# Kernel optimization log

Hardware: AMD Instinct MI355X
Metric: run time of the kernel (lower is better)

The kernel has to match this reference:

```python
import jax, jax.numpy as jnp
import numpy as np

K = 128
HEADS = 8
B = 4
T = 2048


def setup_inputs() -> dict:
    key = jax.random.key(0)
    ks = jax.random.split(key, 6)
    x = jax.random.normal(ks[0], (B, T, K), dtype=jnp.float32)
    s = 1.0 / np.sqrt(K)
    # torch nn.Linear weights are (out_features, in_features)
    Wq = jax.random.uniform(ks[1], (HEADS * K, K), dtype=jnp.float32, minval=-s, maxval=s)
    Wk = jax.random.uniform(ks[2], (HEADS * K, K), dtype=jnp.float32, minval=-s, maxval=s)
    Wv = jax.random.uniform(ks[3], (HEADS * K, K), dtype=jnp.float32, minval=-s, maxval=s)
    su = 1.0 / np.sqrt(HEADS * K)
    Wu = jax.random.uniform(ks[4], (K, HEADS * K), dtype=jnp.float32, minval=-su, maxval=su)
    bu = jax.random.uniform(ks[5], (K,), dtype=jnp.float32, minval=-su, maxval=su)
    return {"x": x, "Wq": Wq, "Wk": Wk, "Wv": Wv, "Wu": Wu, "bu": bu}


def reference(x, Wq, Wk, Wv, Wu, bu):
    b, t, k = x.shape
    h = HEADS
    # project: Linear(k, k*h) then view(b,t,h,k); weight reshaped to (h, k_out, k_in)
    q = jnp.einsum('btk,hdk->bhtd', x, Wq.reshape(h, k, k))
    kk = jnp.einsum('btk,hdk->bhtd', x, Wk.reshape(h, k, k))
    v = jnp.einsum('btk,hdk->bhtd', x, Wv.reshape(h, k, k))
    scale = jnp.asarray(k, x.dtype) ** 0.25
    q = q / scale
    kk = kk / scale
    dot = jnp.einsum('bhtd,bhsd->bhts', q, kk)  # [b,h,t,t]
    att = jax.nn.softmax(dot, axis=-1)
    out = jnp.einsum('bhts,bhsd->bhtd', att, v)  # [b,h,t,k]
    out = out.transpose(0, 2, 1, 3).reshape(b, t, h * k)
    return out @ Wu.T + bu
```

## Files before the change

kernel.cpp:

```cpp
#include <hip/hip_runtime.h>
#include <cmath>

namespace {

constexpr int HEADS = 8;
constexpr int Bn = 4;
constexpr int Tn = 2048;
constexpr int Dn = 128;
constexpr float Q_PRESCALE = 0.1275174340f;

typedef _Float16 half8 __attribute__((ext_vector_type(8)));
typedef _Float16 half4 __attribute__((ext_vector_type(4)));
typedef float f32x4 __attribute__((ext_vector_type(4)));

__global__ __launch_bounds__(256) void cast_kernel(
    const float* __restrict__ x, const float* __restrict__ Wq, const float* __restrict__ Wk,
    const float* __restrict__ Wv, const float* __restrict__ Wu, _Float16* __restrict__ xh,
    _Float16* __restrict__ WH) {
  const int idx = blockIdx.x * 256 + threadIdx.x;
  const size_t base = (size_t)idx * 8;
  const float* src;
  _Float16* dst;
  if (base < 1048576) {
    src = x + base;
    dst = xh + base;
  } else {
    const size_t r = base - 1048576;
    const int s = (int)(r >> 17);
    src = ((s == 0) ? Wq : (s == 1) ? Wk : (s == 2) ? Wv : Wu) + (r & 131071);
    dst = WH + r;
  }
  const float4 a = *reinterpret_cast<const float4*>(src);
  const float4 b = *reinterpret_cast<const float4*>(src + 4);
  half8 h;
  h[0] = (_Float16)a.x; h[1] = (_Float16)a.y; h[2] = (_Float16)a.z; h[3] = (_Float16)a.w;
  h[4] = (_Float16)b.x; h[5] = (_Float16)b.y; h[6] = (_Float16)b.z; h[7] = (_Float16)b.w;
  *reinterpret_cast<half8*>(dst) = h;
}

__global__ __launch_bounds__(256, 4) void proj_kernel(const _Float16* __restrict__ xh,
                                                      const _Float16* __restrict__ WH,
                                                      _Float16* __restrict__ Qh,
                                                      _Float16* __restrict__ Kh,
                                                      _Float16* __restrict__ Vt) {
  __shared__ _Float16 sB[128 * 136];
  const int tid = threadIdx.x;
  const int w = tid >> 6, lane = tid & 63, quad = lane >> 4, l16 = lane & 15;
  const int m0 = blockIdx.x * 128;
  const int n0 = blockIdx.y * 128;

#pragma unroll
  for (int it = 0; it < 8; ++it) {
    const int fid = tid + it * 256;
    const int r = fid >> 4, g = fid & 15;
    const half8 v = *reinterpret_cast<const half8*>(WH + (size_t)(n0 + r) * 128 + g * 8);
    const int p = g ^ (r & 15);
    *reinterpret_cast<half8*>(sB + r * 128 + p * 8) = v;
  }

  half8 af[2][4];
  const _Float16* xp = xh + (size_t)(m0 + w * 32 + l16) * 128 + quad * 8;
#pragma unroll
  for (int mt = 0; mt < 2; ++mt)
#pragma unroll
    for (int kk = 0; kk < 4; ++kk)
      af[mt][kk] = *reinterpret_cast<const half8*>(xp + mt * 16 * 128 + kk * 32);

  __syncthreads();

  f32x4 acc[2][8];
#pragma unroll
  for (int mt = 0; mt < 2; ++mt)
#pragma unroll
    for (int nt = 0; nt < 8; ++nt) acc[mt][nt] = (f32x4){0.f, 0.f, 0.f, 0.f};

#pragma unroll
  for (int kk = 0; kk < 4; ++kk)
#pragma unroll
    for (int nt = 0; nt < 8; ++nt) {
      const int r = nt * 16 + l16;
      const int p = (kk * 4 + quad) ^ l16;
      const half8 bf = *reinterpret_cast<const half8*>(sB + r * 128 + p * 8);
      acc[0][nt] = __builtin_amdgcn_mfma_f32_16x16x32_f16(af[0][kk], bf, acc[0][nt], 0, 0, 0);
      acc[1][nt] = __builtin_amdgcn_mfma_f32_16x16x32_f16(af[1][kk], bf, acc[1][nt], 0, 0, 0);
    }

  const int sel = n0 >> 10;
  const int h = (n0 >> 7) & 7;
  const int b = m0 >> 11;
  const int t0b = m0 & 2047;
  const int bh = b * HEADS + h;
  const float scale = (sel == 0) ? Q_PRESCALE : 1.0f;

  __syncthreads();

  if (sel < 2) {
#pragma unroll
    for (int mt = 0; mt < 2; ++mt)
#pragma unroll
      for (int nt = 0; nt < 8; ++nt)
#pragma unroll
        for (int r = 0; r < 4; ++r)
          sB[(w * 32 + mt * 16 + quad * 4 + r) * 136 + nt * 16 + l16] =
              (_Float16)(acc[mt][nt][r] * scale);
  } else {
#pragma unroll
    for (int mt = 0; mt < 2; ++mt)
#pragma unroll
      for (int nt = 0; nt < 8; ++nt)
#pragma unroll
        for (int r = 0; r < 4; ++r)
          sB[(nt * 16 + l16) * 136 + w * 32 + mt * 16 + quad * 4 + r] = (_Float16)acc[mt][nt][r];
  }
  __syncthreads();

  _Float16* dstbase;
  size_t rstride;
  if (sel == 0) {
    dstbase = Qh + ((size_t)bh * Tn + t0b) * Dn;
    rstride = Dn;
  } else if (sel == 1) {
    dstbase = Kh + ((size_t)bh * Tn + t0b) * Dn;
    rstride = Dn;
  } else {
    dstbase = Vt + ((size_t)bh * Dn) * Tn + t0b;
    rstride = Tn;
  }
#pragma unroll
  for (int it = 0; it < 8; ++it) {
    const int fid = tid + it * 256;
    const int r = fid >> 4, g = fid & 15;
    const half8 v = *reinterpret_cast<const half8*>(sB + r * 136 + g * 8);
    *reinterpret_cast<half8*>(dstbase + (size_t)r * rstride + g * 8) = v;
  }
}

__global__ __launch_bounds__(256, 2) void flash_kernel(const _Float16* __restrict__ Qh,
                                                       const _Float16* __restrict__ Kh,
                                                       const _Float16* __restrict__ Vt,
                                                       _Float16* __restrict__ Obh) {
  __shared__ _Float16 sK[2][64 * 128];
  __shared__ _Float16 sV[2][128 * 64];
  __shared__ _Float16 sP[4][32 * 64];

  const int tid = threadIdx.x;
  const int w = tid >> 6;
  const int lane = tid & 63;
  const int quad = lane >> 4;
  const int l16 = lane & 15;
  const int qt = blockIdx.x;
  const int bh = blockIdx.y;
  constexpr int NT = Tn / 64;

  half8 qf[2][4];
#pragma unroll
  for (int qg = 0; qg < 2; ++qg) {
    const _Float16* Qp =
        Qh + ((size_t)bh * Tn + qt * 128 + w * 32 + qg * 16 + l16) * Dn + quad * 8;
#pragma unroll
    for (int kk = 0; kk < 4; ++kk) qf[qg][kk] = *reinterpret_cast<const half8*>(Qp + kk * 32);
  }

  const _Float16* Kp = Kh + (size_t)bh * Tn * Dn;
  const _Float16* Vp = Vt + (size_t)bh * Dn * Tn;
  _Float16* sPw = sP[w];

  f32x4 o[2][8];
#pragma unroll
  for (int qg = 0; qg < 2; ++qg)
#pragma unroll
    for (int nt = 0; nt < 8; ++nt) o[qg][nt] = (f32x4){0.f, 0.f, 0.f, 0.f};
  float lsum[2] = {0.f, 0.f};

  half8 kreg[4], vreg[4];
  const int kr = tid >> 4, kg = tid & 15;
  const int vr = tid >> 3, vg = tid & 7;

#pragma unroll
  for (int it = 0; it < 4; ++it) {
    kreg[it] = *reinterpret_cast<const half8*>(Kp + (size_t)(kr + it * 16) * Dn + kg * 8);
    vreg[it] = *reinterpret_cast<const half8*>(Vp + (size_t)(vr + it * 32) * Tn + vg * 8);
  }
#pragma unroll
  for (int it = 0; it < 4; ++it) {
    const int r = kr + it * 16;
    const int p = kg ^ (r & 15);
    *reinterpret_cast<half8*>(sK[0] + r * 128 + p * 8) = kreg[it];
    const int rv = vr + it * 32;
    const int pv = vg ^ ((rv & 7) ^ ((rv >> 1) & 4));
    *reinterpret_cast<half8*>(sV[0] + rv * 64 + pv * 8) = vreg[it];
  }
#pragma unroll
  for (int it = 0; it < 4; ++it) {
    kreg[it] = *reinterpret_cast<const half8*>(Kp + (size_t)(64 + kr + it * 16) * Dn + kg * 8);
    vreg[it] = *reinterpret_cast<const half8*>(Vp + (size_t)(vr + it * 32) * Tn + 64 + vg * 8);
  }
  __syncthreads();

  f32x4 s_t[2][4];
#pragma unroll
  for (int qg = 0; qg < 2; ++qg)
#pragma unroll
    for (int j = 0; j < 4; ++j) s_t[qg][j] = (f32x4){0.f, 0.f, 0.f, 0.f};
#pragma unroll
  for (int kk = 0; kk < 4; ++kk)
#pragma unroll
    for (int j = 0; j < 4; ++j) {
      const int p = (kk * 4 + quad) ^ l16;
      const half8 kf = *reinterpret_cast<const half8*>(sK[0] + (j * 16 + l16) * 128 + p * 8);
      s_t[0][j] = __builtin_amdgcn_mfma_f32_16x16x32_f16(kf, qf[0][kk], s_t[0][j], 0, 0, 0);
      s_t[1][j] = __builtin_amdgcn_mfma_f32_16x16x32_f16(kf, qf[1][kk], s_t[1][j], 0, 0, 0);
    }

  for (int st = 0; st < NT; ++st) {
    const int cur = st & 1, nxt = cur ^ 1;

    if (st + 1 < NT) {
#pragma unroll
      for (int it = 0; it < 4; ++it) {
        const int r = kr + it * 16;
        const int p = kg ^ (r & 15);
        *reinterpret_cast<half8*>(sK[nxt] + r * 128 + p * 8) = kreg[it];
        const int rv = vr + it * 32;
        const int pv = vg ^ ((rv & 7) ^ ((rv >> 1) & 4));
        *reinterpret_cast<half8*>(sV[nxt] + rv * 64 + pv * 8) = vreg[it];
      }
    }
    if (st + 2 < NT) {
      const _Float16* knext = Kp + (size_t)(st + 2) * 64 * Dn;
      const _Float16* vnext = Vp + (st + 2) * 64;
#pragma unroll
      for (int it = 0; it < 4; ++it) {
        kreg[it] = *reinterpret_cast<const half8*>(knext + (size_t)(kr + it * 16) * Dn + kg * 8);
        vreg[it] = *reinterpret_cast<const half8*>(vnext + (size_t)(vr + it * 32) * Tn + vg * 8);
      }
    }

#pragma unroll
    for (int h = 0; h < 2; ++h) {
#pragma unroll
      for (int qg = 0; qg < 2; ++qg)
#pragma unroll
        for (int jj = 0; jj < 2; ++jj) {
          const int j = h * 2 + jj;
          f32x4 e;
          e[0] = __builtin_amdgcn_exp2f(s_t[qg][j][0]);
          e[1] = __builtin_amdgcn_exp2f(s_t[qg][j][1]);
          e[2] = __builtin_amdgcn_exp2f(s_t[qg][j][2]);
          e[3] = __builtin_amdgcn_exp2f(s_t[qg][j][3]);
          lsum[qg] += (e[0] + e[1]) + (e[2] + e[3]);
          half4 h4;
          h4[0] = (_Float16)e[0]; h4[1] = (_Float16)e[1];
          h4[2] = (_Float16)e[2]; h4[3] = (_Float16)e[3];
          const int g = j * 2 + (quad >> 1);
          const int p = g ^ (l16 & 7);
          *reinterpret_cast<half4*>(sPw + (qg * 16 + l16) * 64 + p * 8 + (quad & 1) * 4) = h4;
        }
      half8 pf[2];
#pragma unroll
      for (int qg = 0; qg < 2; ++qg) {
        const int pA = (h * 4 + quad) ^ (l16 & 7);
        pf[qg] = *reinterpret_cast<const half8*>(sPw + (qg * 16 + l16) * 64 + pA * 8);
      }
#pragma unroll
      for (int nt = 0; nt < 8; ++nt) {
        const int r = nt * 16 + l16;
        const int pV = (h * 4 + quad) ^ ((r & 7) ^ ((r >> 1) & 4));
        const half8 vf = *reinterpret_cast<const half8*>(sV[cur] + r * 64 + pV * 8);
        o[0][nt] = __builtin_amdgcn_mfma_f32_16x16x32_f16(pf[0], vf, o[0][nt], 0, 0, 0);
        o[1][nt] = __builtin_amdgcn_mfma_f32_16x16x32_f16(pf[1], vf, o[1][nt], 0, 0, 0);
      }
    }

    __syncthreads();

    if (st + 1 < NT) {
#pragma unroll
      for (int qg = 0; qg < 2; ++qg)
#pragma unroll
        for (int j = 0; j < 4; ++j) s_t[qg][j] = (f32x4){0.f, 0.f, 0.f, 0.f};
#pragma unroll
      for (int kk = 0; kk < 4; ++kk)
#pragma unroll
        for (int j = 0; j < 4; ++j) {
          const int p = (kk * 4 + quad) ^ l16;
          const half8 kf =
              *reinterpret_cast<const half8*>(sK[nxt] + (j * 16 + l16) * 128 + p * 8);
          s_t[0][j] = __builtin_amdgcn_mfma_f32_16x16x32_f16(kf, qf[0][kk], s_t[0][j], 0, 0, 0);
          s_t[1][j] = __builtin_amdgcn_mfma_f32_16x16x32_f16(kf, qf[1][kk], s_t[1][j], 0, 0, 0);
        }
    }
  }

  float* sLw = reinterpret_cast<float*>(sPw);
#pragma unroll
  for (int qg = 0; qg < 2; ++qg) {
    float ls = lsum[qg];
    ls += __shfl_xor(ls, 16);
    ls += __shfl_xor(ls, 32);
    if (quad == 0) sLw[qg * 16 + l16] = 1.0f / ls;
  }
  const int b = bh >> 3, h = bh & 7;
#pragma unroll
  for (int qg = 0; qg < 2; ++qg) {
    const f32x4 inv4 = *reinterpret_cast<const f32x4*>(sLw + qg * 16 + quad * 4);
#pragma unroll
    for (int r = 0; r < 4; ++r) {
      const size_t trow =
          (size_t)(b * Tn + qt * 128 + w * 32 + qg * 16 + quad * 4 + r) * (HEADS * Dn);
#pragma unroll
      for (int nt = 0; nt < 8; ++nt)
        Obh[trow + h * Dn + nt * 16 + l16] = (_Float16)(o[qg][nt][r] * inv4[r]);
    }
  }
}

__global__ __launch_bounds__(256, 4) void outproj_kernel(const _Float16* __restrict__ Obh,
                                                         const _Float16* __restrict__ Wuh,
                                                         const float* __restrict__ bu,
                                                         float* __restrict__ out) {
  __shared__ float sR[4 * 32 * 128];
  const int tid = threadIdx.x;
  const int w = tid >> 6, lane = tid & 63, quad = lane >> 4, l16 = lane & 15;
  const int r0 = blockIdx.x * 32;

  f32x4 acc[2][8];
#pragma unroll
  for (int mt = 0; mt < 2; ++mt)
#pragma unroll
    for (int nt = 0; nt < 8; ++nt) acc[mt][nt] = (f32x4){0.f, 0.f, 0.f, 0.f};

  const _Float16* ap = Obh + (size_t)(r0 + l16) * 1024 + w * 256 + quad * 8;
  const _Float16* bp = Wuh + (size_t)l16 * 1024 + w * 256 + quad * 8;

#pragma unroll
  for (int kk = 0; kk < 8; ++kk) {
    const half8 a0 = *reinterpret_cast<const half8*>(ap + kk * 32);
    const half8 a1 = *reinterpret_cast<const half8*>(ap + 16 * 1024 + kk * 32);
#pragma unroll
    for (int nt = 0; nt < 8; ++nt) {
      const half8 bf = *reinterpret_cast<const half8*>(bp + (size_t)nt * 16 * 1024 + kk * 32);
      acc[0][nt] = __builtin_amdgcn_mfma_f32_16x16x32_f16(a0, bf, acc[0][nt], 0, 0, 0);
      acc[1][nt] = __builtin_amdgcn_mfma_f32_16x16x32_f16(a1, bf, acc[1][nt], 0, 0, 0);
    }
  }

#pragma unroll
  for (int mt = 0; mt < 2; ++mt)
#pragma unroll
    for (int nt = 0; nt < 8; ++nt)
#pragma unroll
      for (int r = 0; r < 4; ++r)
        sR[w * 4096 + (mt * 16 + quad * 4 + r) * 128 + nt * 16 + l16] = acc[mt][nt][r];
  __syncthreads();

#pragma unroll
  for (int it = 0; it < 16; ++it) {
    const int idx = tid + it * 256;
    const int row = idx >> 7, col = idx & 127;
    const float v = sR[idx] + sR[4096 + idx] + sR[8192 + idx] + sR[12288 + idx] + bu[col];
    out[(size_t)(r0 + row) * Dn + col] = v;
  }
}

}

extern "C" void kernel_launch(void* const* d_in, const int* in_sizes, int n_in, void* d_out,
                              int out_size, void* d_ws, size_t ws_size, hipStream_t stream) {
  (void)in_sizes; (void)n_in; (void)out_size; (void)ws_size;
  const float* x = (const float*)d_in[0];
  const float* Wq = (const float*)d_in[1];
  const float* Wk = (const float*)d_in[2];
  const float* Wv = (const float*)d_in[3];
  const float* Wu = (const float*)d_in[4];
  const float* bu = (const float*)d_in[5];
  float* out = (float*)d_out;

  constexpr size_t NE = (size_t)Bn * HEADS * Tn * Dn;
  char* ws = (char*)d_ws;
  _Float16* xh = (_Float16*)ws;
  _Float16* WH = (_Float16*)(ws + 2097152);
  _Float16* Qh = (_Float16*)(ws + 4194304);
  _Float16* Kh = (_Float16*)(ws + 4194304 + NE * 2);
  _Float16* Vt = (_Float16*)(ws + 4194304 + NE * 4);
  _Float16* Obh = (_Float16*)(ws + 4194304 + NE * 6);
  _Float16* Wuh = WH + 393216;

  cast_kernel<<<dim3(768), 256, 0, stream>>>(x, Wq, Wk, Wv, Wu, xh, WH);
  proj_kernel<<<dim3(64, 24), 256, 0, stream>>>(xh, WH, Qh, Kh, Vt);
  flash_kernel<<<dim3(16, 32), 256, 0, stream>>>(Qh, Kh, Vt, Obh);
  outproj_kernel<<<dim3(256), 256, 0, stream>>>(Obh, Wuh, bu, out);
}
```

Before: 168.5 us.

## Switch flash attention to 32x32 MFMA with register-resident P and larger Q tiles

Rewrites the flash attention kernel to use 32x32x16 MFMA instead of 16x16x32. Each wave now owns 64 query rows (256 per block), so the grid halves to 256 blocks. The softmax probabilities are packed straight into MFMA B-operand registers, which removes the LDS round trip for P. The output is staged through swizzled LDS so it can be written to global memory as coalesced 16-byte stores. In exchange there is more register pressure (launch bounds drop to one block per SM) and fewer blocks to hide latency, which could cost occupancy and load balance on a large GPU.

```diff
diff --git a/kernel.cpp b/kernel.cpp
--- a/kernel.cpp
+++ b/kernel.cpp
@@ -11,7 +11,11 @@
 
 typedef _Float16 half8 __attribute__((ext_vector_type(8)));
 typedef _Float16 half4 __attribute__((ext_vector_type(4)));
+typedef _Float16 half2v __attribute__((ext_vector_type(2)));
 typedef float f32x4 __attribute__((ext_vector_type(4)));
+typedef float f32x16 __attribute__((ext_vector_type(16)));
+typedef unsigned int u32;
+typedef unsigned int u32x4 __attribute__((ext_vector_type(4)));
 
 __global__ __launch_bounds__(256) void cast_kernel(
     const float* __restrict__ x, const float* __restrict__ Wq, const float* __restrict__ Wk,
@@ -135,60 +139,68 @@
   }
 }
 
-__global__ __launch_bounds__(256, 2) void flash_kernel(const _Float16* __restrict__ Qh,
+__global__ __launch_bounds__(256, 1) void flash_kernel(const _Float16* __restrict__ Qh,
                                                        const _Float16* __restrict__ Kh,
                                                        const _Float16* __restrict__ Vt,
                                                        _Float16* __restrict__ Obh) {
-  __shared__ _Float16 sK[2][64 * 128];
-  __shared__ _Float16 sV[2][128 * 64];
-  __shared__ _Float16 sP[4][32 * 64];
+  __shared__ _Float16 sAll[32768];
 
   const int tid = threadIdx.x;
   const int w = tid >> 6;
   const int lane = tid & 63;
-  const int quad = lane >> 4;
-  const int l16 = lane & 15;
+  const int l31 = lane & 31;
+  const int h = lane >> 5;
   const int qt = blockIdx.x;
   const int bh = blockIdx.y;
   constexpr int NT = Tn / 64;
 
-  half8 qf[2][4];
-#pragma unroll
-  for (int qg = 0; qg < 2; ++qg) {
+  half8 qf[2][8];
+#pragma unroll
+  for (int qb = 0; qb < 2; ++qb) {
     const _Float16* Qp =
-        Qh + ((size_t)bh * Tn + qt * 128 + w * 32 + qg * 16 + l16) * Dn + quad * 8;
-#pragma unroll
-    for (int kk = 0; kk < 4; ++kk) qf[qg][kk] = *reinterpret_cast<const half8*>(Qp + kk * 32);
+        Qh + ((size_t)bh * Tn + qt * 256 + w * 64 + qb * 32 + l31) * Dn + h * 8;
+#pragma unroll
+    for (int ds = 0; ds < 8; ++ds) qf[qb][ds] = *reinterpret_cast<const half8*>(Qp + ds * 16);
   }
 
   const _Float16* Kp = Kh + (size_t)bh * Tn * Dn;
   const _Float16* Vp = Vt + (size_t)bh * Dn * Tn;
-  _Float16* sPw = sP[w];
-
-  f32x4 o[2][8];
-#pragma unroll
-  for (int qg = 0; qg < 2; ++qg)
-#pragma unroll
-    for (int nt = 0; nt < 8; ++nt) o[qg][nt] = (f32x4){0.f, 0.f, 0.f, 0.f};
+
+  f32x16 o[4][2];
+#pragma unroll
+  for (int db = 0; db < 4; ++db)
+#pragma unroll
+    for (int qb = 0; qb < 2; ++qb) o[db][qb] = (f32x16)(0.f);
   float lsum[2] = {0.f, 0.f};
 
   half8 kreg[4], vreg[4];
   const int kr = tid >> 4, kg = tid & 15;
   const int vr = tid >> 3, vg = tid & 7;
+  const int vG = (vg >> 1) * 2;
+  const int vO = (vg & 1) * 4;
 
 #pragma unroll
   for (int it = 0; it < 4; ++it) {
     kreg[it] = *reinterpret_cast<const half8*>(Kp + (size_t)(kr + it * 16) * Dn + kg * 8);
     vreg[it] = *reinterpret_cast<const half8*>(Vp + (size_t)(vr + it * 32) * Tn + vg * 8);
   }
-#pragma unroll
-  for (int it = 0; it < 4; ++it) {
-    const int r = kr + it * 16;
-    const int p = kg ^ (r & 15);
-    *reinterpret_cast<half8*>(sK[0] + r * 128 + p * 8) = kreg[it];
-    const int rv = vr + it * 32;
-    const int pv = vg ^ ((rv & 7) ^ ((rv >> 1) & 4));
-    *reinterpret_cast<half8*>(sV[0] + rv * 64 + pv * 8) = vreg[it];
+  {
+    _Float16* sK0 = sAll;
+    _Float16* sV0 = sAll + 16384;
+#pragma unroll
+    for (int it = 0; it < 4; ++it) {
+      const int r = kr + it * 16;
+      const int p = kg ^ (r & 15);
+      *reinterpret_cast<half8*>(sK0 + r * 128 + p * 8) = kreg[it];
+      const int rv = vr + it * 32;
+      const int sw = (rv & 7) ^ ((rv >> 1) & 4);
+      const half8 v = vreg[it];
+      half4 lo, hi;
+      lo[0] = v[0]; lo[1] = v[1]; lo[2] = v[2]; lo[3] = v[3];
+      hi[0] = v[4]; hi[1] = v[5]; hi[2] = v[6]; hi[3] = v[7];
+      *reinterpret_cast<half4*>(sV0 + rv * 64 + ((vG ^ sw) * 8) + vO) = lo;
+      *reinterpret_cast<half4*>(sV0 + rv * 64 + (((vG + 1) ^ sw) * 8) + vO) = hi;
+    }
   }
 #pragma unroll
   for (int it = 0; it < 4; ++it) {
@@ -197,33 +209,48 @@
   }
   __syncthreads();
 
-  f32x4 s_t[2][4];
-#pragma unroll
-  for (int qg = 0; qg < 2; ++qg)
-#pragma unroll
-    for (int j = 0; j < 4; ++j) s_t[qg][j] = (f32x4){0.f, 0.f, 0.f, 0.f};
-#pragma unroll
-  for (int kk = 0; kk < 4; ++kk)
-#pragma unroll
-    for (int j = 0; j < 4; ++j) {
-      const int p = (kk * 4 + quad) ^ l16;
-      const half8 kf = *reinterpret_cast<const half8*>(sK[0] + (j * 16 + l16) * 128 + p * 8);
-      s_t[0][j] = __builtin_amdgcn_mfma_f32_16x16x32_f16(kf, qf[0][kk], s_t[0][j], 0, 0, 0);
-      s_t[1][j] = __builtin_amdgcn_mfma_f32_16x16x32_f16(kf, qf[1][kk], s_t[1][j], 0, 0, 0);
-    }
+  f32x16 sacc[2][2];
+#pragma unroll
+  for (int qb = 0; qb < 2; ++qb)
+#pragma unroll
+    for (int kb = 0; kb < 2; ++kb) sacc[qb][kb] = (f32x16)(0.f);
+#pragma unroll
+  for (int ds = 0; ds < 8; ++ds) {
+    half8 kf[2];
+#pragma unroll
+    for (int kb = 0; kb < 2; ++kb) {
+      const int r = kb * 32 + l31;
+      const int p = (ds * 2 + h) ^ (r & 15);
+      kf[kb] = *reinterpret_cast<const half8*>(sAll + r * 128 + p * 8);
+    }
+#pragma unroll
+    for (int qb = 0; qb < 2; ++qb)
+#pragma unroll
+      for (int kb = 0; kb < 2; ++kb)
+        sacc[qb][kb] =
+            __builtin_amdgcn_mfma_f32_32x32x16_f16(kf[kb], qf[qb][ds], sacc[qb][kb], 0, 0, 0);
+  }
 
   for (int st = 0; st < NT; ++st) {
     const int cur = st & 1, nxt = cur ^ 1;
+    _Float16* sKn = sAll + nxt * 8192;
+    _Float16* sVn = sAll + 16384 + nxt * 8192;
+    _Float16* sVc = sAll + 16384 + cur * 8192;
 
     if (st + 1 < NT) {
 #pragma unroll
       for (int it = 0; it < 4; ++it) {
         const int r = kr + it * 16;
         const int p = kg ^ (r & 15);
-        *reinterpret_cast<half8*>(sK[nxt] + r * 128 + p * 8) = kreg[it];
+        *reinterpret_cast<half8*>(sKn + r * 128 + p * 8) = kreg[it];
         const int rv = vr + it * 32;
-        const int pv = vg ^ ((rv & 7) ^ ((rv >> 1) & 4));
-        *reinterpret_cast<half8*>(sV[nxt] + rv * 64 + pv * 8) = vreg[it];
+        const int sw = (rv & 7) ^ ((rv >> 1) & 4);
+        const half8 v = vreg[it];
+        half4 lo, hi;
+        lo[0] = v[0]; lo[1] = v[1]; lo[2] = v[2]; lo[3] = v[3];
+        hi[0] = v[4]; hi[1] = v[5]; hi[2] = v[6]; hi[3] = v[7];
+        *reinterpret_cast<half4*>(sVn + rv * 64 + ((vG ^ sw) * 8) + vO) = lo;
+        *reinterpret_cast<half4*>(sVn + rv * 64 + (((vG + 1) ^ sw) * 8) + vO) = hi;
       }
     }
     if (st + 2 < NT) {
@@ -236,39 +263,38 @@
       }
     }
 
-#pragma unroll
-    for (int h = 0; h < 2; ++h) {
-#pragma unroll
-      for (int qg = 0; qg < 2; ++qg)
-#pragma unroll
-        for (int jj = 0; jj < 2; ++jj) {
-          const int j = h * 2 + jj;
-          f32x4 e;
-          e[0] = __builtin_amdgcn_exp2f(s_t[qg][j][0]);
-          e[1] = __builtin_amdgcn_exp2f(s_t[qg][j][1]);
-          e[2] = __builtin_amdgcn_exp2f(s_t[qg][j][2]);
-          e[3] = __builtin_amdgcn_exp2f(s_t[qg][j][3]);
-          lsum[qg] += (e[0] + e[1]) + (e[2] + e[3]);
-          half4 h4;
-          h4[0] = (_Float16)e[0]; h4[1] = (_Float16)e[1];
-          h4[2] = (_Float16)e[2]; h4[3] = (_Float16)e[3];
-          const int g = j * 2 + (quad >> 1);
-          const int p = g ^ (l16 & 7);
-          *reinterpret_cast<half4*>(sPw + (qg * 16 + l16) * 64 + p * 8 + (quad & 1) * 4) = h4;
+    half8 bfr[2][4];
+#pragma unroll
+    for (int qb = 0; qb < 2; ++qb) {
+#pragma unroll
+      for (int kb = 0; kb < 2; ++kb) {
+        u32 pk[8];
+        float part = 0.f;
+#pragma unroll
+        for (int j = 0; j < 8; ++j) {
+          const float e0 = __builtin_amdgcn_exp2f(sacc[qb][kb][2 * j]);
+          const float e1 = __builtin_amdgcn_exp2f(sacc[qb][kb][2 * j + 1]);
+          part += e0 + e1;
+          half2v hp = {(_Float16)e0, (_Float16)e1};
+          pk[j] = __builtin_bit_cast(u32, hp);
         }
-      half8 pf[2];
-#pragma unroll
-      for (int qg = 0; qg < 2; ++qg) {
-        const int pA = (h * 4 + quad) ^ (l16 & 7);
-        pf[qg] = *reinterpret_cast<const half8*>(sPw + (qg * 16 + l16) * 64 + pA * 8);
-      }
-#pragma unroll
-      for (int nt = 0; nt < 8; ++nt) {
-        const int r = nt * 16 + l16;
-        const int pV = (h * 4 + quad) ^ ((r & 7) ^ ((r >> 1) & 4));
-        const half8 vf = *reinterpret_cast<const half8*>(sV[cur] + r * 64 + pV * 8);
-        o[0][nt] = __builtin_amdgcn_mfma_f32_16x16x32_f16(pf[0], vf, o[0][nt], 0, 0, 0);
-        o[1][nt] = __builtin_amdgcn_mfma_f32_16x16x32_f16(pf[1], vf, o[1][nt], 0, 0, 0);
+        lsum[qb] += part;
+        u32x4 beven = {pk[0], pk[1], pk[2], pk[3]};
+        u32x4 bodd = {pk[4], pk[5], pk[6], pk[7]};
+        bfr[qb][kb * 2] = __builtin_bit_cast(half8, beven);
+        bfr[qb][kb * 2 + 1] = __builtin_bit_cast(half8, bodd);
+      }
+    }
+
+#pragma unroll
+    for (int kb16 = 0; kb16 < 4; ++kb16) {
+#pragma unroll
+      for (int db = 0; db < 4; ++db) {
+        const int r = db * 32 + l31;
+        const int pv = (kb16 * 2 + h) ^ ((r & 7) ^ ((r >> 1) & 4));
+        const half8 vf = *reinterpret_cast<const half8*>(sVc + r * 64 + pv * 8);
+        o[db][0] = __builtin_amdgcn_mfma_f32_32x32x16_f16(vf, bfr[0][kb16], o[db][0], 0, 0, 0);
+        o[db][1] = __builtin_amdgcn_mfma_f32_32x32x16_f16(vf, bfr[1][kb16], o[db][1], 0, 0, 0);
       }
     }
 
@@ -276,46 +302,66 @@
 
     if (st + 1 < NT) {
 #pragma unroll
-      for (int qg = 0; qg < 2; ++qg)
-#pragma unroll
-        for (int j = 0; j < 4; ++j) s_t[qg][j] = (f32x4){0.f, 0.f, 0.f, 0.f};
-#pragma unroll
-      for (int kk = 0; kk < 4; ++kk)
-#pragma unroll
-        for (int j = 0; j < 4; ++j) {
-          const int p = (kk * 4 + quad) ^ l16;
-          const half8 kf =
-              *reinterpret_cast<const half8*>(sK[nxt] + (j * 16 + l16) * 128 + p * 8);
-          s_t[0][j] = __builtin_amdgcn_mfma_f32_16x16x32_f16(kf, qf[0][kk], s_t[0][j], 0, 0, 0);
-          s_t[1][j] = __builtin_amdgcn_mfma_f32_16x16x32_f16(kf, qf[1][kk], s_t[1][j], 0, 0, 0);
+      for (int qb = 0; qb < 2; ++qb)
+#pragma unroll
+        for (int kb = 0; kb < 2; ++kb) sacc[qb][kb] = (f32x16)(0.f);
+#pragma unroll
+      for (int ds = 0; ds < 8; ++ds) {
+        half8 kf[2];
+#pragma unroll
+        for (int kb = 0; kb < 2; ++kb) {
+          const int r = kb * 32 + l31;
+          const int p = (ds * 2 + h) ^ (r & 15);
+          kf[kb] = *reinterpret_cast<const half8*>(sKn + r * 128 + p * 8);
         }
-    }
-  }
-
-  float* sLw = reinterpret_cast<float*>(sPw);
-#pragma unroll
-  for (int qg = 0; qg < 2; ++qg) {
-    float ls = lsum[qg];
-    ls += __shfl_xor(ls, 16);
+#pragma unroll
+        for (int qb = 0; qb < 2; ++qb)
+#pragma unroll
+          for (int kb = 0; kb < 2; ++kb)
+            sacc[qb][kb] =
+                __builtin_amdgcn_mfma_f32_32x32x16_f16(kf[kb], qf[qb][ds], sacc[qb][kb], 0, 0, 0);
+      }
+    }
+  }
+
+  float inv[2];
+#pragma unroll
+  for (int qb = 0; qb < 2; ++qb) {
+    float ls = lsum[qb];
     ls += __shfl_xor(ls, 32);
-    if (quad == 0) sLw[qg * 16 + l16] = 1.0f / ls;
-  }
-  const int b = bh >> 3, h = bh & 7;
-#pragma unroll
-  for (int qg = 0; qg < 2; ++qg) {
-    const f32x4 inv4 = *reinterpret_cast<const f32x4*>(sLw + qg * 16 + quad * 4);
-#pragma unroll
-    for (int r = 0; r < 4; ++r) {
-      const size_t trow =
-          (size_t)(b * Tn + qt * 128 + w * 32 + qg * 16 + quad * 4 + r) * (HEADS * Dn);
-#pragma unroll
-      for (int nt = 0; nt < 8; ++nt)
-        Obh[trow + h * Dn + nt * 16 + l16] = (_Float16)(o[qg][nt][r] * inv4[r]);
-    }
-  }
-}
-
-__global__ __launch_bounds__(256, 4) void outproj_kernel(const _Float16* __restrict__ Obh,
+    inv[qb] = 1.0f / ls;
+  }
+
+  __syncthreads();
+  _Float16* const sO = sAll + w * 8192;
+
+#pragma unroll
+  for (int qb = 0; qb < 2; ++qb) {
+    const int qrow = qb * 32 + l31;
+#pragma unroll
+    for (int db = 0; db < 4; ++db)
+#pragma unroll
+      for (int grp = 0; grp < 4; ++grp) {
+        const int d0 = db * 32 + grp * 8 + h * 4;
+        half4 hv;
+#pragma unroll
+        for (int i = 0; i < 4; ++i) hv[i] = (_Float16)(o[db][qb][grp * 4 + i] * inv[qb]);
+        const int idx = qrow * 128 + (((d0 >> 3) ^ (qrow & 15)) << 3) + (d0 & 7);
+        *reinterpret_cast<half4*>(sO + idx) = hv;
+      }
+  }
+  const int b = bh >> 3, hh = bh & 7;
+#pragma unroll
+  for (int it = 0; it < 16; ++it) {
+    const int idx = lane + it * 64;
+    const int row = idx >> 4, g = idx & 15;
+    const half8 v = *reinterpret_cast<const half8*>(sO + row * 128 + ((g ^ (row & 15)) << 3));
+    const size_t t = (size_t)(b * Tn + qt * 256 + w * 64 + row);
+    *reinterpret_cast<half8*>(Obh + t * (HEADS * Dn) + hh * 128 + g * 8) = v;
+  }
+}
+
+__global__ __launch_bounds__(256, 2) void outproj_kernel(const _Float16* __restrict__ Obh,
                                                          const _Float16* __restrict__ Wuh,
                                                          const float* __restrict__ bu,
                                                          float* __restrict__ out) {
@@ -388,6 +434,6 @@
 
   cast_kernel<<<dim3(768), 256, 0, stream>>>(x, Wq, Wk, Wv, Wu, xh, WH);
   proj_kernel<<<dim3(64, 24), 256, 0, stream>>>(xh, WH, Qh, Kh, Vt);
-  flash_kernel<<<dim3(16, 32), 256, 0, stream>>>(Qh, Kh, Vt, Obh);
+  flash_kernel<<<dim3(8, 32), 256, 0, stream>>>(Qh, Kh, Vt, Obh);
   outproj_kernel<<<dim3(256), 256, 0, stream>>>(Obh, Wuh, bu, out);
 }
```

After: 172.7 us. +2.5%, slower.
